# Optimization experiments

Measured on AMD Instinct MI355X. Metric: run time of the kernel, lower is better.

The kernel has to match this reference:

```python
import jax, jax.numpy as jnp
import numpy as np

MARGIN = 0.5
EPS = 1e-6  # torch F.pairwise_distance eps, added to the difference


def _make_indices(B, seed=0):
    rng = np.random.default_rng(seed)
    i1 = np.empty(B, dtype=np.int64)
    i2 = np.empty(B, dtype=np.int64)
    for i in range(B):
        a, b = rng.choice(B, size=2, replace=False)
        while a == i or b == i:
            a, b = rng.choice(B, size=2, replace=False)
        i1[i], i2[i] = a, b
    return i1, i2


def setup_inputs() -> dict:
    key = jax.random.key(0)
    k1, k2 = jax.random.split(key)
    B, D = 8192, 4096
    features = jax.random.normal(k1, (B, D), dtype=jnp.float32)
    label = jax.random.uniform(k2, (B, 1), dtype=jnp.float32) * 200.0  # bone-age-like months
    i1, i2 = _make_indices(B)
    return {
        "features": features,
        "label": label,
        "idx1": jnp.asarray(i1),
        "idx2": jnp.asarray(i2),
    }


def reference(features, label, idx1, idx2):
    # features: [B, D], label: [B, 1]
    a = features
    t1 = features[idx1]                                   # [B, D]
    t2 = features[idx2]                                   # [B, D]
    # L1Loss(reduction='sum') on per-sample labels
    d1 = jnp.sum(jnp.abs(label - label[idx1]), axis=-1)   # [B]
    d2 = jnp.sum(jnp.abs(label - label[idx2]), axis=-1)   # [B]
    # if d1 >= d2: near = t2, far = t1 else near = t1, far = t2
    swap = (d1 >= d2)[:, None]
    near = jnp.where(swap, t2, t1)
    far = jnp.where(swap, t1, t2)
    # TripletMarginLoss(margin=0.5, p=2); per-sample inputs are 1-D vectors,
    # so each call's 'mean' reduction is over a single element (identity).
    dn = jnp.sqrt(jnp.sum((a - near + EPS) ** 2, axis=-1))  # [B]
    df = jnp.sqrt(jnp.sum((a - far + EPS) ** 2, axis=-1))   # [B]
    per_sample = jnp.maximum(dn - df + MARGIN, 0.0)
    # loss is always >= 0, so the `if loss >= 0` accumulates every sample.
    return jnp.sum(per_sample)
```

## Files before the change

kernel.cpp:

```cpp
#include <hip/hip_runtime.h>

#define FEAT_D 4096
#define MARGIN_F 0.5f
#define EPS_F 1e-6f
#define ROWS_PER_BLK 4


__global__ __launch_bounds__(256) void triplet_loss_kernel(
    const float* __restrict__ features,
    const float* __restrict__ label,
    const int* __restrict__ idx1,
    const int* __restrict__ idx2,
    float* __restrict__ partials)
{
    const int tid = threadIdx.x;
    const int row0 = blockIdx.x * ROWS_PER_BLK;

    __shared__ float sh1[ROWS_PER_BLK][4], sh2[ROWS_PER_BLK][4];

    float4 bufA[12], bufB[12];

#define ISSUE(BUF, R)                                                          \
    {                                                                          \
        const int rr_ = (R);                                                   \
        const int j1_ = idx1[rr_], j2_ = idx2[rr_];                            \
        const float4* pa_ = reinterpret_cast<const float4*>(features + (size_t)rr_ * FEAT_D) + tid; \
        const float4* p1_ = reinterpret_cast<const float4*>(features + (size_t)j1_ * FEAT_D) + tid; \
        const float4* p2_ = reinterpret_cast<const float4*>(features + (size_t)j2_ * FEAT_D) + tid; \
        _Pragma("unroll")                                                      \
        for (int k = 0; k < 4; ++k) BUF[k]     = pa_[k * 256];                 \
        _Pragma("unroll")                                                      \
        for (int k = 0; k < 4; ++k) BUF[4 + k] = p1_[k * 256];                 \
        _Pragma("unroll")                                                      \
        for (int k = 0; k < 4; ++k) BUF[8 + k] = p2_[k * 256];                 \
    }                                                                          \
    __builtin_amdgcn_sched_barrier(0);

#define COMPUTE(BUF, SLOT)                                                     \
    {                                                                          \
        float s1_ = 0.f, s2_ = 0.f;                                            \
        _Pragma("unroll")                                                      \
        for (int k = 0; k < 4; ++k) {                                          \
            float d_;                                                          \
            d_ = BUF[k].x - BUF[4+k].x + EPS_F; s1_ += d_ * d_;                \
            d_ = BUF[k].y - BUF[4+k].y + EPS_F; s1_ += d_ * d_;                \
            d_ = BUF[k].z - BUF[4+k].z + EPS_F; s1_ += d_ * d_;                \
            d_ = BUF[k].w - BUF[4+k].w + EPS_F; s1_ += d_ * d_;                \
            d_ = BUF[k].x - BUF[8+k].x + EPS_F; s2_ += d_ * d_;                \
            d_ = BUF[k].y - BUF[8+k].y + EPS_F; s2_ += d_ * d_;                \
            d_ = BUF[k].z - BUF[8+k].z + EPS_F; s2_ += d_ * d_;                \
            d_ = BUF[k].w - BUF[8+k].w + EPS_F; s2_ += d_ * d_;                \
        }                                                                      \
        _Pragma("unroll")                                                      \
        for (int off = 32; off > 0; off >>= 1) {                               \
            s1_ += __shfl_down(s1_, off, 64);                                  \
            s2_ += __shfl_down(s2_, off, 64);                                  \
        }                                                                      \
        if ((tid & 63) == 0) { sh1[SLOT][tid >> 6] = s1_; sh2[SLOT][tid >> 6] = s2_; } \
    }

    ISSUE(bufA, row0)
    ISSUE(bufB, row0 + 1)
    COMPUTE(bufA, 0)
    ISSUE(bufA, row0 + 2)
    COMPUTE(bufB, 1)
    ISSUE(bufB, row0 + 3)
    COMPUTE(bufA, 2)
    COMPUTE(bufB, 3)

    __syncthreads();

    if (tid < ROWS_PER_BLK) {
        const int r = row0 + tid;
        const float S1 = sh1[tid][0] + sh1[tid][1] + sh1[tid][2] + sh1[tid][3];
        const float S2 = sh2[tid][0] + sh2[tid][1] + sh2[tid][2] + sh2[tid][3];
        const float lab = label[r];
        const float d1 = fabsf(lab - label[idx1[r]]);
        const float d2 = fabsf(lab - label[idx2[r]]);
        const bool swap = (d1 >= d2);
        const float sn = swap ? S2 : S1;
        const float sf = swap ? S1 : S2;
        partials[r] = fmaxf(sqrtf(sn) - sqrtf(sf) + MARGIN_F, 0.f);
    }
#undef ISSUE
#undef COMPUTE
}

__global__ __launch_bounds__(1024) void reduce_kernel(
    const float* __restrict__ partials, float* __restrict__ out, int n)
{
    const int tid = threadIdx.x;
    float s = 0.f;
    const float4* p4 = reinterpret_cast<const float4*>(partials);
    for (int i = tid; i < n / 4; i += 1024) {
        const float4 v = p4[i];
        s += (v.x + v.y) + (v.z + v.w);
    }
#pragma unroll
    for (int off = 32; off > 0; off >>= 1)
        s += __shfl_down(s, off, 64);

    __shared__ float sh[16];
    const int wave = tid >> 6;
    const int lane = tid & 63;
    if (lane == 0) sh[wave] = s;
    __syncthreads();
    if (tid == 0) {
        float t = 0.f;
#pragma unroll
        for (int w = 0; w < 16; ++w) t += sh[w];
        out[0] = t;
    }
}

extern "C" void kernel_launch(void* const* d_in, const int* in_sizes, int n_in,
                              void* d_out, int out_size, void* d_ws, size_t ws_size,
                              hipStream_t stream) {
    const float* features = (const float*)d_in[0];
    const float* label    = (const float*)d_in[1];
    const int*   idx1     = (const int*)d_in[2];
    const int*   idx2     = (const int*)d_in[3];
    float* out      = (float*)d_out;
    float* partials = (float*)d_ws;

    const int B = in_sizes[1];

    triplet_loss_kernel<<<B / ROWS_PER_BLK, 256, 0, stream>>>(features, label, idx1, idx2, partials);
    reduce_kernel<<<1, 1024, 0, stream>>>(partials, out, B);
}
```

Baseline: 63.38 us.

## Double rows per block and reduce per-block losses via strided atomic slots

Each block now handles eight rows, keeping the double-buffered register pipeline running across more rows. It sums its per-row losses in shared memory and atomically adds the total into one of 64 padded global slots, replacing the per-row partials array. A tiny 64-thread kernel then reduces the slots, and a memset zeroes them first. Halving the grid lowers occupancy parallelism, the memset adds a launch, and float atomics make the summation order nondeterministic.

```diff
diff --git a/kernel.cpp b/kernel.cpp
--- a/kernel.cpp
+++ b/kernel.cpp
@@ -3,20 +3,22 @@
 #define FEAT_D 4096
 #define MARGIN_F 0.5f
 #define EPS_F 1e-6f
-#define ROWS_PER_BLK 4
-
+#define ROWS_PER_BLK 8
+#define NSLOT 64
+#define SLOT_STRIDE 32
 
 __global__ __launch_bounds__(256) void triplet_loss_kernel(
     const float* __restrict__ features,
     const float* __restrict__ label,
     const int* __restrict__ idx1,
     const int* __restrict__ idx2,
-    float* __restrict__ partials)
+    float* __restrict__ accum)
 {
     const int tid = threadIdx.x;
     const int row0 = blockIdx.x * ROWS_PER_BLK;
 
     __shared__ float sh1[ROWS_PER_BLK][4], sh2[ROWS_PER_BLK][4];
+    __shared__ float shl[ROWS_PER_BLK];
 
     float4 bufA[12], bufB[12];
 
@@ -66,7 +68,15 @@
     COMPUTE(bufB, 1)
     ISSUE(bufB, row0 + 3)
     COMPUTE(bufA, 2)
+    ISSUE(bufA, row0 + 4)
     COMPUTE(bufB, 3)
+    ISSUE(bufB, row0 + 5)
+    COMPUTE(bufA, 4)
+    ISSUE(bufA, row0 + 6)
+    COMPUTE(bufB, 5)
+    ISSUE(bufB, row0 + 7)
+    COMPUTE(bufA, 6)
+    COMPUTE(bufB, 7)
 
     __syncthreads();
 
@@ -80,37 +90,29 @@
         const bool swap = (d1 >= d2);
         const float sn = swap ? S2 : S1;
         const float sf = swap ? S1 : S2;
-        partials[r] = fmaxf(sqrtf(sn) - sqrtf(sf) + MARGIN_F, 0.f);
+        shl[tid] = fmaxf(sqrtf(sn) - sqrtf(sf) + MARGIN_F, 0.f);
+    }
+    __syncthreads();
+
+    if (tid == 0) {
+        float t = 0.f;
+#pragma unroll
+        for (int r = 0; r < ROWS_PER_BLK; ++r) t += shl[r];
+        atomicAdd(&accum[(blockIdx.x & (NSLOT - 1)) * SLOT_STRIDE], t);
     }
 #undef ISSUE
 #undef COMPUTE
 }
 
-__global__ __launch_bounds__(1024) void reduce_kernel(
-    const float* __restrict__ partials, float* __restrict__ out, int n)
+__global__ __launch_bounds__(64) void final_reduce_kernel(
+    const float* __restrict__ accum, float* __restrict__ out)
 {
-    const int tid = threadIdx.x;
-    float s = 0.f;
-    const float4* p4 = reinterpret_cast<const float4*>(partials);
-    for (int i = tid; i < n / 4; i += 1024) {
-        const float4 v = p4[i];
-        s += (v.x + v.y) + (v.z + v.w);
-    }
+    const int lane = threadIdx.x;
+    float s = accum[lane * SLOT_STRIDE];
 #pragma unroll
     for (int off = 32; off > 0; off >>= 1)
         s += __shfl_down(s, off, 64);
-
-    __shared__ float sh[16];
-    const int wave = tid >> 6;
-    const int lane = tid & 63;
-    if (lane == 0) sh[wave] = s;
-    __syncthreads();
-    if (tid == 0) {
-        float t = 0.f;
-#pragma unroll
-        for (int w = 0; w < 16; ++w) t += sh[w];
-        out[0] = t;
-    }
+    if (lane == 0) out[0] = s;
 }
 
 extern "C" void kernel_launch(void* const* d_in, const int* in_sizes, int n_in,
@@ -120,11 +122,12 @@
     const float* label    = (const float*)d_in[1];
     const int*   idx1     = (const int*)d_in[2];
     const int*   idx2     = (const int*)d_in[3];
-    float* out      = (float*)d_out;
-    float* partials = (float*)d_ws;
+    float* out   = (float*)d_out;
+    float* accum = (float*)d_ws;
 
     const int B = in_sizes[1];
 
-    triplet_loss_kernel<<<B / ROWS_PER_BLK, 256, 0, stream>>>(features, label, idx1, idx2, partials);
-    reduce_kernel<<<1, 1024, 0, stream>>>(partials, out, B);
+    hipMemsetAsync(accum, 0, NSLOT * SLOT_STRIDE * sizeof(float), stream);
+    triplet_loss_kernel<<<B / ROWS_PER_BLK, 256, 0, stream>>>(features, label, idx1, idx2, accum);
+    final_reduce_kernel<<<1, 64, 0, stream>>>(accum, out);
 }
```

Measured after the change: 69.77 us. +10.1%, slower.
